# Kernel optimization log

Measured on AMD Instinct MI355X. Metric: run time of the kernel, lower is better.

## Reference

```python
import jax, jax.numpy as jnp
import numpy as np


def _conv(x, w, b, stride, pad):
    y = jax.lax.conv_general_dilated(
        x, w, (stride, stride), [(pad, pad), (pad, pad)],
        dimension_numbers=('NCHW', 'OIHW', 'NCHW'))
    return y + b[None, :, None, None]


def _maxpool(x):
    # kernel 3, stride 2, padding 1 (torch MaxPool2d semantics)
    return jax.lax.reduce_window(
        x, -jnp.inf, jax.lax.max,
        (1, 1, 3, 3), (1, 1, 2, 2), [(0, 0), (0, 0), (1, 1), (1, 1)])


def _squash(s, eps=1e-8):
    n2 = jnp.sum(s * s, axis=-1, keepdims=True)
    return s * (n2 / (1.0 + n2)) / jnp.sqrt(n2 + eps)


def setup_inputs() -> dict:
    key = jax.random.key(0)
    ks = jax.random.split(key, 17)
    s = 0.05
    inp = {
        'x': jax.random.normal(ks[0], (128, 3, 32, 32), jnp.float32),
        'cw1': jax.random.normal(ks[1], (96, 3, 3, 3), jnp.float32) * s,
        'cb1': jnp.zeros((96,), jnp.float32),
        'cw2': jax.random.normal(ks[2], (256, 96, 3, 3), jnp.float32) * s,
        'cb2': jnp.zeros((256,), jnp.float32),
        'cw3': jax.random.normal(ks[3], (384, 256, 3, 3), jnp.float32) * s,
        'cb3': jnp.zeros((384,), jnp.float32),
        'pw': jax.random.normal(ks[4], (256, 384, 3, 3), jnp.float32) * s,  # 32 caps * 8 dim
        'pb': jnp.zeros((256,), jnp.float32),
        'Wcaps': jax.random.normal(ks[5], (100, 1152, 16, 8), jnp.float32) * s,
        'fw1': jax.random.normal(ks[6], (1600, 4096), jnp.float32) * s,
        'fb1': jnp.zeros((4096,), jnp.float32),
        'fw2': jax.random.normal(ks[7], (4096, 4096), jnp.float32) * s,
        'fb2': jnp.zeros((4096,), jnp.float32),
        'fw3': jax.random.normal(ks[8], (4096, 100), jnp.float32) * s,
        'fb3': jnp.zeros((100,), jnp.float32),
    }
    return inp


def reference(x, cw1, cb1, cw2, cb2, cw3, cb3, pw, pb, Wcaps,
              fw1, fb1, fw2, fb2, fw3, fb3):
    ROUTINGS = 3
    # AlexNet-style conv backbone
    h = jax.nn.relu(_conv(x, cw1, cb1, 1, 1))   # [B,96,32,32]
    h = _maxpool(h)                              # [B,96,16,16]
    h = jax.nn.relu(_conv(h, cw2, cb2, 1, 1))   # [B,256,16,16]
    h = _maxpool(h)                              # [B,256,8,8]
    h = jax.nn.relu(_conv(h, cw3, cb3, 1, 1))   # [B,384,8,8]
    # PrimaryCaps: conv 384 -> 32*8, k3 s1 p0 -> [B,256,6,6]
    p = _conv(h, pw, pb, 1, 0)
    u = _squash(p.reshape(p.shape[0], -1, 8))   # [B,1152,8]
    # DenseCapsule: x_hat[b,o,i,d] = sum_e W[o,i,d,e] * u[b,i,e]
    x_hat = jnp.einsum('oide,bie->boid', Wcaps, u)  # [B,100,1152,16]
    x_hat_d = jax.lax.stop_gradient(x_hat)
    b = jnp.zeros(x_hat.shape[:3], x_hat.dtype)     # [B,100,1152]
    v = None
    for r in range(ROUTINGS):
        c = jax.nn.softmax(b, axis=1)               # couple over out caps
        if r == ROUTINGS - 1:
            v = _squash(jnp.einsum('boi,boid->bod', c, x_hat))
        else:
            v = _squash(jnp.einsum('boi,boid->bod', c, x_hat_d))
            b = b + jnp.einsum('boid,bod->boi', x_hat_d, v)
    # Flatten + FC head (dropout is identity at eval)
    f = v.reshape(v.shape[0], -1)                   # [B,1600]
    f = jax.nn.relu(f @ fw1 + fb1)
    f = jax.nn.relu(f @ fw2 + fb2)
    return f @ fw3 + fb3                            # [B,100]
```

## Files before the change

kernel.cpp:

```cpp
#include <hip/hip_runtime.h>
#include <cstddef>


typedef __attribute__((ext_vector_type(8))) short bf8_t;
typedef __attribute__((ext_vector_type(4))) float f4_t;

__device__ inline void cvt_hilo8(const float* f, unsigned* h, unsigned* l)
{
  #pragma unroll
  for (int j = 0; j < 4; ++j) {
    unsigned u0 = __float_as_uint(f[2 * j]);
    unsigned u1 = __float_as_uint(f[2 * j + 1]);
    h[j] = (u0 >> 16) | (u1 & 0xFFFF0000u);
    float r0 = f[2 * j]     - __uint_as_float(u0 & 0xFFFF0000u);
    float r1 = f[2 * j + 1] - __uint_as_float(u1 & 0xFFFF0000u);
    l[j] = (__float_as_uint(r0) >> 16) | (__float_as_uint(r1) & 0xFFFF0000u);
  }
}

__device__ inline void split1(float f, unsigned short& h, unsigned short& l)
{
  unsigned u = __float_as_uint(f);
  h = (unsigned short)(u >> 16);
  float r = f - __uint_as_float(u & 0xFFFF0000u);
  l = (unsigned short)(__float_as_uint(r) >> 16);
}

__device__ inline float bf2f(unsigned short h, unsigned short l)
{
  return __uint_as_float((unsigned)h << 16) + __uint_as_float((unsigned)l << 16);
}

__global__ __launch_bounds__(256) void wsplit_k(
    const float* __restrict__ w, unsigned short* __restrict__ oh,
    unsigned short* __restrict__ ol, int CO, int CI)
{
  int idx = blockIdx.x * 256 + threadIdx.x;
  int ci = idx % CI;
  int t2 = idx / CI;
  int r = t2 % 9, co = t2 / 9;
  float f = w[((size_t)co * CI + ci) * 9 + r];
  unsigned short h, l;
  split1(f, h, l);
  oh[idx] = h; ol[idx] = l;
}

__global__ __launch_bounds__(256) void conv1_k(
    const float* __restrict__ x, const float* __restrict__ wt,
    const float* __restrict__ bias, unsigned short* __restrict__ oh,
    unsigned short* __restrict__ ol)
{
  int idx = blockIdx.x * 256 + threadIdx.x;
  int w = idx & 31, h = (idx >> 5) & 31, b = idx >> 10;
  int co0 = blockIdx.y * 24;

  float xv[27];
  const float* xb = x + (size_t)b * 3072;
  #pragma unroll
  for (int ci = 0; ci < 3; ++ci)
    #pragma unroll
    for (int dh = 0; dh < 3; ++dh) {
      int ih = h + dh - 1;
      #pragma unroll
      for (int dw = 0; dw < 3; ++dw) {
        int iw = w + dw - 1;
        bool ok = ((unsigned)ih < 32u) & ((unsigned)iw < 32u);
        xv[ci * 9 + dh * 3 + dw] = ok ? xb[(ci << 10) + (ih << 5) + iw] : 0.f;
      }
    }

  size_t obase = ((size_t)b * 1024 + (h << 5) + w) * 96 + co0;
  const float* wp = wt + (size_t)co0 * 27;
  #pragma unroll 2
  for (int cp = 0; cp < 12; ++cp) {
    float a0 = bias[co0 + 2 * cp], a1 = bias[co0 + 2 * cp + 1];
    #pragma unroll
    for (int k = 0; k < 27; ++k) {
      a0 += xv[k] * wp[(2 * cp) * 27 + k];
      a1 += xv[k] * wp[(2 * cp + 1) * 27 + k];
    }
    a0 = fmaxf(a0, 0.f); a1 = fmaxf(a1, 0.f);
    unsigned short h0, l0, h1, l1;
    split1(a0, h0, l0); split1(a1, h1, l1);
    *(unsigned*)(oh + obase + 2 * cp) = (unsigned)h0 | ((unsigned)h1 << 16);
    *(unsigned*)(ol + obase + 2 * cp) = (unsigned)l0 | ((unsigned)l1 << 16);
  }
}

template <int C, int H>
__global__ __launch_bounds__(256) void maxpool_bf(
    const unsigned short* __restrict__ inh, const unsigned short* __restrict__ inl,
    unsigned short* __restrict__ outh, unsigned short* __restrict__ outl)
{
  constexpr int Ho = H >> 1;
  int idx = blockIdx.x * 256 + threadIdx.x;
  int c = idx % C;
  int q = idx / C;
  int wo = q % Ho;
  int q2 = q / Ho;
  int ho = q2 % Ho, b = q2 / Ho;
  float best = -3.4e38f;
  unsigned short bh = 0, bl = 0;
  #pragma unroll
  for (int dh = 0; dh < 3; ++dh) {
    int ih = 2 * ho - 1 + dh;
    if ((unsigned)ih >= (unsigned)H) continue;
    #pragma unroll
    for (int dw = 0; dw < 3; ++dw) {
      int iw = 2 * wo - 1 + dw;
      if ((unsigned)iw >= (unsigned)H) continue;
      size_t off = ((size_t)(b * H + ih) * H + iw) * C + c;
      unsigned short uh = inh[off], ul = inl[off];
      float f = bf2f(uh, ul);
      if (f > best) { best = f; bh = uh; bl = ul; }
    }
  }
  outh[idx] = bh; outl[idx] = bl;
}

template <int CI, int H, int PAD, int WO, bool SPLIT>
__global__ __launch_bounds__(256) void convgemm_nhwc(
    const unsigned short* __restrict__ inh, const unsigned short* __restrict__ inl,
    const unsigned short* __restrict__ wh, const unsigned short* __restrict__ wl,
    const float* __restrict__ bias, unsigned short* __restrict__ outh,
    unsigned short* __restrict__ outl, float* __restrict__ outf,
    int CO, int relu, int KC)
{
  constexpr int K = CI * 9;
  constexpr int NPIX = WO * WO;
  __shared__ uint4 Ah[256], Al[256], Bh[256], Bl[256];
  int n0 = blockIdx.x * 64, m0 = blockIdx.y * 64;
  int kbeg = SPLIT ? blockIdx.z * KC : 0;
  int kend = SPLIT ? kbeg + KC : K;
  int t = threadIdx.x;
  int lane = t & 63;
  int wave = __builtin_amdgcn_readfirstlane(t >> 6);
  int wm = wave & 1, wn = wave >> 1;
  int lr = lane & 15, lq = lane >> 4;

  int nn = m0 + lane;
  int bpix = nn / NPIX, xy = nn - bpix * NPIX;
  int ho = xy / WO, wo = xy - ho * WO;
  int ih0 = ho - PAD, iw0 = wo - PAD;
  size_t ibase = (size_t)bpix * H * H;

  uint4 a_h, a_l, b_h, b_l;
  auto loadA = [&](int k0) {
    int kk = k0 + wave * 8;
    int r = kk / CI, ci0 = kk - r * CI;
    int dh = r / 3, dw = r - dh * 3;
    int ih = ih0 + dh, iw = iw0 + dw;
    bool ok = ((unsigned)ih < (unsigned)H) & ((unsigned)iw < (unsigned)H);
    if (ok) {
      size_t ad = ((ibase + (size_t)ih * H + iw) * CI + ci0);
      a_h = *(const uint4*)(inh + ad);
      a_l = *(const uint4*)(inl + ad);
    } else {
      a_h = make_uint4(0u, 0u, 0u, 0u);
      a_l = make_uint4(0u, 0u, 0u, 0u);
    }
  };
  auto loadB = [&](int k0) {
    int kk = k0 + wave * 8;
    size_t ad = (size_t)(n0 + lane) * K + kk;
    b_h = *(const uint4*)(wh + ad);
    b_l = *(const uint4*)(wl + ad);
  };

  loadA(kbeg); loadB(kbeg);
  f4_t acc[2][2];
  #pragma unroll
  for (int mt = 0; mt < 2; ++mt)
    #pragma unroll
    for (int nt = 0; nt < 2; ++nt) acc[mt][nt] = (f4_t)0.0f;

  for (int k0 = kbeg; k0 < kend; k0 += 32) {
    if (k0 > kbeg) __syncthreads();
    Ah[t] = a_h; Al[t] = a_l; Bh[t] = b_h; Bl[t] = b_l;
    __syncthreads();
    if (k0 + 32 < kend) { loadA(k0 + 32); loadB(k0 + 32); }
    bf8_t av_h[2], av_l[2], bv_h[2], bv_l[2];
    #pragma unroll
    for (int mt = 0; mt < 2; ++mt) {
      int ui = lq * 64 + wm * 32 + mt * 16 + lr;
      av_h[mt] = *(const bf8_t*)&Ah[ui];
      av_l[mt] = *(const bf8_t*)&Al[ui];
    }
    #pragma unroll
    for (int nt = 0; nt < 2; ++nt) {
      int ui = lq * 64 + wn * 32 + nt * 16 + lr;
      bv_h[nt] = *(const bf8_t*)&Bh[ui];
      bv_l[nt] = *(const bf8_t*)&Bl[ui];
    }
    #pragma unroll
    for (int mt = 0; mt < 2; ++mt)
      #pragma unroll
      for (int nt = 0; nt < 2; ++nt) {
        acc[mt][nt] = __builtin_amdgcn_mfma_f32_16x16x32_bf16(av_h[mt], bv_h[nt], acc[mt][nt], 0, 0, 0);
        acc[mt][nt] = __builtin_amdgcn_mfma_f32_16x16x32_bf16(av_h[mt], bv_l[nt], acc[mt][nt], 0, 0, 0);
        acc[mt][nt] = __builtin_amdgcn_mfma_f32_16x16x32_bf16(av_l[mt], bv_h[nt], acc[mt][nt], 0, 0, 0);
      }
  }
  #pragma unroll
  for (int mt = 0; mt < 2; ++mt)
    #pragma unroll
    for (int nt = 0; nt < 2; ++nt) {
      #pragma unroll
      for (int r = 0; r < 4; ++r) {
        int m = m0 + wm * 32 + mt * 16 + lq * 4 + r;
        int n = n0 + wn * 32 + nt * 16 + lr;
        size_t oidx = (size_t)m * CO + n;
        if (SPLIT) {
          atomicAdd(outf + oidx, acc[mt][nt][r]);
        } else {
          float vv = acc[mt][nt][r] + bias[n];
          if (relu) vv = fmaxf(vv, 0.f);
          unsigned short h, l;
          split1(vv, h, l);
          outh[oidx] = h; outl[oidx] = l;
        }
      }
    }
}

__global__ __launch_bounds__(256) void fc_mfma(
    const float* __restrict__ A, const float* __restrict__ W,
    float* __restrict__ C, int K, int N, int KC)
{
  __shared__ uint4 Ah[256], Al[256], Bh[256], Bl[256];
  int n0 = blockIdx.x * 64, m0 = blockIdx.y * 64;
  int kbeg = blockIdx.z * KC, kend = kbeg + KC;
  int t = threadIdx.x;
  int lane = t & 63;
  int wave = __builtin_amdgcn_readfirstlane(t >> 6);
  int wm = wave & 1, wn = wave >> 1;
  int lr = lane & 15, lq = lane >> 4;
  int smA = t >> 2, sgA = t & 3;

  float fa[8], fb[8];
  auto loadA = [&](int k0) {
    const float4* ap = (const float4*)(A + (size_t)(m0 + smA) * K + k0 + sgA * 8);
    float4 a0 = ap[0], a1 = ap[1];
    fa[0] = a0.x; fa[1] = a0.y; fa[2] = a0.z; fa[3] = a0.w;
    fa[4] = a1.x; fa[5] = a1.y; fa[6] = a1.z; fa[7] = a1.w;
  };
  auto loadB = [&](int k0) {
    const float* wp = W + (size_t)(k0 + wave * 8) * N + n0 + lane;
    #pragma unroll
    for (int j = 0; j < 8; ++j) fb[j] = wp[(size_t)j * N];
  };

  loadA(kbeg); loadB(kbeg);
  f4_t acc[2][2];
  #pragma unroll
  for (int mt = 0; mt < 2; ++mt)
    #pragma unroll
    for (int nt = 0; nt < 2; ++nt) acc[mt][nt] = (f4_t)0.0f;

  for (int k0 = kbeg; k0 < kend; k0 += 32) {
    if (k0 > kbeg) __syncthreads();
    unsigned ha[4], la[4], hb[4], lb[4];
    cvt_hilo8(fa, ha, la);
    cvt_hilo8(fb, hb, lb);
    Ah[sgA * 64 + smA] = make_uint4(ha[0], ha[1], ha[2], ha[3]);
    Al[sgA * 64 + smA] = make_uint4(la[0], la[1], la[2], la[3]);
    Bh[wave * 64 + lane] = make_uint4(hb[0], hb[1], hb[2], hb[3]);
    Bl[wave * 64 + lane] = make_uint4(lb[0], lb[1], lb[2], lb[3]);
    __syncthreads();
    if (k0 + 32 < kend) { loadA(k0 + 32); loadB(k0 + 32); }
    bf8_t av_h[2], av_l[2], bv_h[2], bv_l[2];
    #pragma unroll
    for (int mt = 0; mt < 2; ++mt) {
      int ui = lq * 64 + wm * 32 + mt * 16 + lr;
      av_h[mt] = *(const bf8_t*)&Ah[ui];
      av_l[mt] = *(const bf8_t*)&Al[ui];
    }
    #pragma unroll
    for (int nt = 0; nt < 2; ++nt) {
      int ui = lq * 64 + wn * 32 + nt * 16 + lr;
      bv_h[nt] = *(const bf8_t*)&Bh[ui];
      bv_l[nt] = *(const bf8_t*)&Bl[ui];
    }
    #pragma unroll
    for (int mt = 0; mt < 2; ++mt)
      #pragma unroll
      for (int nt = 0; nt < 2; ++nt) {
        acc[mt][nt] = __builtin_amdgcn_mfma_f32_16x16x32_bf16(av_h[mt], bv_h[nt], acc[mt][nt], 0, 0, 0);
        acc[mt][nt] = __builtin_amdgcn_mfma_f32_16x16x32_bf16(av_h[mt], bv_l[nt], acc[mt][nt], 0, 0, 0);
        acc[mt][nt] = __builtin_amdgcn_mfma_f32_16x16x32_bf16(av_l[mt], bv_h[nt], acc[mt][nt], 0, 0, 0);
      }
  }
  #pragma unroll
  for (int mt = 0; mt < 2; ++mt)
    #pragma unroll
    for (int nt = 0; nt < 2; ++nt) {
      #pragma unroll
      for (int r = 0; r < 4; ++r) {
        int m = m0 + wm * 32 + mt * 16 + lq * 4 + r;
        int n = n0 + wn * 32 + nt * 16 + lr;
        atomicAdd(C + (size_t)m * N + n, acc[mt][nt][r]);
      }
    }
}

__global__ __launch_bounds__(256) void squash8_k(
    const float* __restrict__ p, const float* __restrict__ pb,
    float* __restrict__ ut)
{
  int idx = blockIdx.x * 256 + threadIdx.x;
  if (idx >= 147456) return;
  int b = idx & 127, i = idx >> 7;
  float pv[8];
  #pragma unroll
  for (int e = 0; e < 8; ++e) {
    int f = i * 8 + e;
    int co = f / 36, pix = f - co * 36;
    pv[e] = p[((size_t)b * 36 + pix) * 256 + co] + pb[co];
  }
  float n2 = 0.f;
  #pragma unroll
  for (int e = 0; e < 8; ++e) n2 += pv[e] * pv[e];
  float sc = (n2 / (1.f + n2)) * rsqrtf(n2 + 1e-8f);
  #pragma unroll
  for (int e = 0; e < 8; ++e)
    ut[(size_t)i * 1024 + e * 128 + b] = pv[e] * sc;
}

__global__ __launch_bounds__(256) void caps_squash16(
    const float* __restrict__ s, float* __restrict__ v, float* __restrict__ vt)
{
  int idx = blockIdx.x * 256 + threadIdx.x;
  if (idx >= 12800) return;
  int b = idx / 100, o = idx % 100;
  const float4* sp = (const float4*)(s + (size_t)idx * 16);
  float4 a = sp[0], bb = sp[1], c = sp[2], d = sp[3];
  float n2 = a.x * a.x + a.y * a.y + a.z * a.z + a.w * a.w +
             bb.x * bb.x + bb.y * bb.y + bb.z * bb.z + bb.w * bb.w +
             c.x * c.x + c.y * c.y + c.z * c.z + c.w * c.w +
             d.x * d.x + d.y * d.y + d.z * d.z + d.w * d.w;
  float sc = (n2 / (1.f + n2)) * rsqrtf(n2 + 1e-8f);
  float vv[16] = {a.x, a.y, a.z, a.w, bb.x, bb.y, bb.z, bb.w,
                  c.x, c.y, c.z, c.w, d.x, d.y, d.z, d.w};
  float4* vp = (float4*)(v + (size_t)idx * 16);
  float4 o0 = {vv[0] * sc, vv[1] * sc, vv[2] * sc, vv[3] * sc};
  float4 o1 = {vv[4] * sc, vv[5] * sc, vv[6] * sc, vv[7] * sc};
  float4 o2 = {vv[8] * sc, vv[9] * sc, vv[10] * sc, vv[11] * sc};
  float4 o3 = {vv[12] * sc, vv[13] * sc, vv[14] * sc, vv[15] * sc};
  vp[0] = o0; vp[1] = o1; vp[2] = o2; vp[3] = o3;
  #pragma unroll
  for (int dd = 0; dd < 16; ++dd)
    vt[((size_t)o * 16 + dd) * 128 + b] = vv[dd] * sc;
}

__global__ __launch_bounds__(256) void caps_spass_mfma(
    const float* __restrict__ W, const float* __restrict__ ut,
    const float* __restrict__ ct, float* __restrict__ s, int uniform)
{
  __shared__ uint4 Ah[512], Al[512];
  int o = blockIdx.x, ks = blockIdx.y;
  int t = threadIdx.x;
  int lane = t & 63;
  int wave = __builtin_amdgcn_readfirstlane(t >> 6);
  int lr = lane & 15, lq = lane >> 4;
  int b = t & 127, half = t >> 7;
  int i0 = ks * 144;

  float fu[16], fc[2], fw[8];
  auto loadUC = [&](int j) {
    int ib = i0 + j * 4 + half * 2;
    #pragma unroll
    for (int q = 0; q < 2; ++q) {
      int i = ib + q;
      #pragma unroll
      for (int e = 0; e < 8; ++e)
        fu[q * 8 + e] = ut[(size_t)i * 1024 + e * 128 + b];
      fc[q] = uniform ? 0.01f : ct[((size_t)o * 1152 + i) * 128 + b];
    }
  };
  auto loadW = [&](int j) {
    int i = i0 + j * 4 + lq;
    const float4* wp = (const float4*)(W + (((size_t)o * 1152 + i) * 16 + lr) * 8);
    float4 w0 = wp[0], w1 = wp[1];
    fw[0] = w0.x; fw[1] = w0.y; fw[2] = w0.z; fw[3] = w0.w;
    fw[4] = w1.x; fw[5] = w1.y; fw[6] = w1.z; fw[7] = w1.w;
  };

  loadUC(0); loadW(0);
  f4_t acc[2];
  acc[0] = (f4_t)0.0f; acc[1] = (f4_t)0.0f;

  for (int j = 0; j < 36; ++j) {
    float cu[16];
    #pragma unroll
    for (int q = 0; q < 2; ++q)
      #pragma unroll
      for (int e = 0; e < 8; ++e)
        cu[q * 8 + e] = fc[q] * fu[q * 8 + e];
    unsigned h0[4], l0[4], h1[4], l1[4], wh[4], wl[4];
    cvt_hilo8(cu, h0, l0);
    cvt_hilo8(cu + 8, h1, l1);
    cvt_hilo8(fw, wh, wl);
    uint4 uwh = make_uint4(wh[0], wh[1], wh[2], wh[3]);
    uint4 uwl = make_uint4(wl[0], wl[1], wl[2], wl[3]);
    bf8_t bfh = *(const bf8_t*)&uwh;
    bf8_t bfl = *(const bf8_t*)&uwl;
    if (j > 0) __syncthreads();
    Ah[(half * 2 + 0) * 128 + b] = make_uint4(h0[0], h0[1], h0[2], h0[3]);
    Al[(half * 2 + 0) * 128 + b] = make_uint4(l0[0], l0[1], l0[2], l0[3]);
    Ah[(half * 2 + 1) * 128 + b] = make_uint4(h1[0], h1[1], h1[2], h1[3]);
    Al[(half * 2 + 1) * 128 + b] = make_uint4(l1[0], l1[1], l1[2], l1[3]);
    __syncthreads();
    if (j + 1 < 36) { loadUC(j + 1); loadW(j + 1); }
    #pragma unroll
    for (int mt = 0; mt < 2; ++mt) {
      int bidx = wave * 16 + mt * 64 + lr;
      bf8_t avh = *(const bf8_t*)&Ah[lq * 128 + bidx];
      bf8_t avl = *(const bf8_t*)&Al[lq * 128 + bidx];
      acc[mt] = __builtin_amdgcn_mfma_f32_16x16x32_bf16(avh, bfh, acc[mt], 0, 0, 0);
      acc[mt] = __builtin_amdgcn_mfma_f32_16x16x32_bf16(avh, bfl, acc[mt], 0, 0, 0);
      acc[mt] = __builtin_amdgcn_mfma_f32_16x16x32_bf16(avl, bfh, acc[mt], 0, 0, 0);
    }
  }
  #pragma unroll
  for (int mt = 0; mt < 2; ++mt)
    #pragma unroll
    for (int r = 0; r < 4; ++r) {
      int bb = wave * 16 + mt * 64 + lq * 4 + r;
      atomicAdd(s + ((size_t)bb * 100 + o) * 16 + lr, acc[mt][r]);
    }
}

__global__ __launch_bounds__(256) void caps_bupdate(
    const float* __restrict__ W, const float* __restrict__ ut,
    const float* __restrict__ vt, float* __restrict__ blogt, int accum)
{
  __shared__ __align__(16) float Wt[64 * 160];
  int o = blockIdx.x, ic = blockIdx.y;
  int t = threadIdx.x;
  int lane = t & 63;
  int wave = __builtin_amdgcn_readfirstlane(t >> 6);
  int lr = lane & 15, lq = lane >> 4;
  int dhalf = (lq & 1) << 3;
  int hl = lq >> 1;

  {
    const float4* Wg = (const float4*)(W + ((size_t)o * 1152 + (size_t)ic * 64) * 128);
    for (int l = t; l < 2048; l += 256) {
      float4 w = Wg[l];
      int li = l >> 5;
      int rem = l & 31;
      int d = rem >> 1;
      int e0 = (rem & 1) << 2;
      float* dst = &Wt[li * 160 + e0 * 20 + d];
      dst[0] = w.x; dst[20] = w.y; dst[40] = w.z; dst[60] = w.w;
    }
  }

  bf8_t B1[8], B2[8];
  #pragma unroll
  for (int nt = 0; nt < 8; ++nt) {
    int b = nt * 16 + lr;
    float vv[8];
    #pragma unroll
    for (int j = 0; j < 8; ++j)
      vv[j] = vt[((size_t)o * 16 + dhalf + j) * 128 + b];
    unsigned h[4], l2[4];
    cvt_hilo8(vv, h, l2);
    uint4 uh = make_uint4(h[0], h[1], h[2], h[3]);
    uint4 ul = (lq < 2) ? make_uint4(l2[0], l2[1], l2[2], l2[3])
                        : make_uint4(0u, 0u, 0u, 0u);
    B1[nt] = *(const bf8_t*)&uh;
    B2[nt] = *(const bf8_t*)&ul;
  }
  __syncthreads();

  unsigned lomask = hl ? 0xFFFF0000u : 0u;

  for (int mi = 0; mi < 8; ++mi) {
    int mt = wave * 8 + mi;
    int liA = mt * 2 + (lr >> 3);
    int eA = lr & 7;
    const float* wp = &Wt[liA * 160 + eA * 20 + dhalf];
    float4 wa = *(const float4*)wp;
    float4 wb = *(const float4*)(wp + 4);
    float fw[8] = {wa.x, wa.y, wa.z, wa.w, wb.x, wb.y, wb.z, wb.w};
    unsigned ha[4];
    #pragma unroll
    for (int j = 0; j < 4; ++j) {
      float f0 = fw[2 * j], f1 = fw[2 * j + 1];
      f0 -= __uint_as_float(__float_as_uint(f0) & lomask);
      f1 -= __uint_as_float(__float_as_uint(f1) & lomask);
      ha[j] = (__float_as_uint(f0) >> 16) | (__float_as_uint(f1) & 0xFFFF0000u);
    }
    uint4 ua = make_uint4(ha[0], ha[1], ha[2], ha[3]);
    bf8_t A = *(const bf8_t*)&ua;

    int gi = ic * 64 + mt * 2 + hl;
    const float* up = ut + (size_t)gi * 1024 + (size_t)(((lq & 1) << 2)) * 128;
    #pragma unroll
    for (int nt = 0; nt < 8; ++nt) {
      f4_t acc = (f4_t)0.0f;
      acc = __builtin_amdgcn_mfma_f32_16x16x32_bf16(A, B1[nt], acc, 0, 0, 0);
      acc = __builtin_amdgcn_mfma_f32_16x16x32_bf16(A, B2[nt], acc, 0, 0, 0);
      int b = nt * 16 + lr;
      float p = acc[0] * up[b] + acc[1] * up[128 + b] +
                acc[2] * up[256 + b] + acc[3] * up[384 + b];
      p += __shfl_xor(p, 16);
      if (!(lq & 1)) {
        size_t off = ((size_t)o * 1152 + gi) * 128 + b;
        if (accum) blogt[off] += p; else blogt[off] = p;
      }
    }
  }
}

__global__ __launch_bounds__(256) void caps_softmax(
    const float* __restrict__ blogt, float* __restrict__ ct)
{
  int idx = blockIdx.x * 256 + threadIdx.x;
  if (idx >= 147456) return;
  const float* bp = blogt + idx;
  float m = -3.4e38f;
  for (int o = 0; o < 100; ++o) m = fmaxf(m, bp[(size_t)o * 147456]);
  float sum = 0.f;
  for (int o = 0; o < 100; ++o) sum += __expf(bp[(size_t)o * 147456] - m);
  float inv = 1.f / sum;
  for (int o = 0; o < 100; ++o)
    ct[(size_t)o * 147456 + idx] = __expf(bp[(size_t)o * 147456] - m) * inv;
}

__global__ __launch_bounds__(256) void bias_act_k(
    float* __restrict__ C, const float* __restrict__ bias, int N, int total, int relu)
{
  int idx = blockIdx.x * 256 + threadIdx.x;
  if (idx >= total) return;
  float vv = C[idx] + bias[idx % N];
  if (relu) vv = fmaxf(vv, 0.f);
  C[idx] = vv;
}

__global__ __launch_bounds__(128) void fc3_seed(
    const float* __restrict__ bias, float* __restrict__ out)
{
  int idx = blockIdx.x * 128 + threadIdx.x;
  if (idx < 12800) out[idx] = bias[idx % 100];
}

__global__ __launch_bounds__(128) void fc3_sk(
    const float* __restrict__ A, const float* __restrict__ W,
    float* __restrict__ out)
{
  __shared__ float Al[1024];
  int m = blockIdx.x, z = blockIdx.y, t = threadIdx.x;
  int kbeg = z * 1024;
  const float* ap = A + (size_t)m * 4096 + kbeg;
  for (int l = t; l < 1024; l += 128) Al[l] = ap[l];
  __syncthreads();
  if (t < 100) {
    float acc = 0.f;
    const float* wp = W + (size_t)kbeg * 100 + t;
    #pragma unroll 8
    for (int k = 0; k < 1024; ++k) acc += Al[k] * wp[(size_t)k * 100];
    atomicAdd(out + m * 100 + t, acc);
  }
}

extern "C" void kernel_launch(void* const* d_in, const int* in_sizes, int n_in,
                              void* d_out, int out_size, void* d_ws, size_t ws_size,
                              hipStream_t stream)
{
  (void)in_sizes; (void)n_in; (void)out_size; (void)ws_size;
  const float* x   = (const float*)d_in[0];
  const float* cw1 = (const float*)d_in[1];
  const float* cb1 = (const float*)d_in[2];
  const float* cw2 = (const float*)d_in[3];
  const float* cb2 = (const float*)d_in[4];
  const float* cw3 = (const float*)d_in[5];
  const float* cb3 = (const float*)d_in[6];
  const float* pw  = (const float*)d_in[7];
  const float* pb  = (const float*)d_in[8];
  const float* Wc  = (const float*)d_in[9];
  const float* fw1 = (const float*)d_in[10];
  const float* fb1 = (const float*)d_in[11];
  const float* fw2 = (const float*)d_in[12];
  const float* fb2 = (const float*)d_in[13];
  const float* fw3 = (const float*)d_in[14];
  const float* fb3 = (const float*)d_in[15];
  float* ws = (float*)d_ws;

  const size_t OFF_A  = 0;
  const size_t OFF_B  = 12582912;
  const size_t OFF_U  = 15728640;
  const size_t OFF_P  = 16908288;
  const size_t OFF_C  = 18087936;
  const size_t OFF_V  = 32833536;
  const size_t OFF_S  = 33038336;
  const size_t OFF_F1 = 33243136;
  const size_t OFF_F2 = 33767424;

  float* ut    = ws + OFF_U;
  float* p     = ws + OFF_P;
  float* vt    = ws + OFF_P;
  float* ct    = ws + OFF_C;
  float* v     = ws + OFF_V;
  float* s     = ws + OFF_S;
  float* f1    = ws + OFF_F1;
  float* f2    = ws + OFF_F2;
  float* blogt = ws + OFF_A;

  unsigned short* h1h  = (unsigned short*)(ws + OFF_A);
  unsigned short* h1l  = h1h + 12582912;
  unsigned short* mp1h = (unsigned short*)(ws + OFF_B);
  unsigned short* mp1l = mp1h + 3145728;
  unsigned short* h2h  = (unsigned short*)(ws + OFF_A);
  unsigned short* h2l  = h2h + 8388608;
  unsigned short* mp2h = (unsigned short*)(ws + OFF_B);
  unsigned short* mp2l = mp2h + 2097152;
  unsigned short* h3h  = (unsigned short*)(ws + OFF_A);
  unsigned short* h3l  = h3h + 3145728;

  unsigned short* wc2h = (unsigned short*)(ws + OFF_C);
  unsigned short* wc2l = wc2h + 221184;
  unsigned short* wc3h = wc2l + 221184;
  unsigned short* wc3l = wc3h + 884736;
  unsigned short* pwth = wc3l + 884736;
  unsigned short* pwtl = pwth + 884736;

  hipMemsetAsync(p,  0, (size_t)1179648 * 4, stream);
  hipMemsetAsync(f1, 0, (size_t)524288 * 4, stream);
  hipMemsetAsync(f2, 0, (size_t)524288 * 4, stream);

  wsplit_k<<<864, 256, 0, stream>>>(cw2, wc2h, wc2l, 256, 96);
  wsplit_k<<<3456, 256, 0, stream>>>(cw3, wc3h, wc3l, 384, 256);
  wsplit_k<<<3456, 256, 0, stream>>>(pw,  pwth, pwtl, 256, 384);

  conv1_k<<<dim3(512, 4), 256, 0, stream>>>(x, cw1, cb1, h1h, h1l);
  maxpool_bf<96, 32><<<12288, 256, 0, stream>>>(h1h, h1l, mp1h, mp1l);
  convgemm_nhwc<96, 16, 1, 16, false><<<dim3(4, 512), 256, 0, stream>>>(
      mp1h, mp1l, wc2h, wc2l, cb2, h2h, h2l, nullptr, 256, 1, 0);
  maxpool_bf<256, 16><<<8192, 256, 0, stream>>>(h2h, h2l, mp2h, mp2l);
  convgemm_nhwc<256, 8, 1, 8, false><<<dim3(6, 128), 256, 0, stream>>>(
      mp2h, mp2l, wc3h, wc3l, cb3, h3h, h3l, nullptr, 384, 1, 0);
  convgemm_nhwc<384, 8, 0, 6, true><<<dim3(4, 72, 2), 256, 0, stream>>>(
      h3h, h3l, pwth, pwtl, pb, nullptr, nullptr, p, 256, 0, 1728);
  squash8_k<<<576, 256, 0, stream>>>(p, pb, ut);

  for (int r = 0; r < 3; ++r) {
    hipMemsetAsync(s, 0, (size_t)204800 * 4, stream);
    if (r == 0) {
      caps_spass_mfma<<<dim3(100, 8), 256, 0, stream>>>(Wc, ut, ut , s, 1);
    } else {
      caps_softmax<<<576, 256, 0, stream>>>(blogt, ct);
      caps_spass_mfma<<<dim3(100, 8), 256, 0, stream>>>(Wc, ut, ct, s, 0);
    }
    caps_squash16<<<50, 256, 0, stream>>>(s, v, vt);
    if (r < 2)
      caps_bupdate<<<dim3(100, 18), 256, 0, stream>>>(Wc, ut, vt, blogt, r);
  }

  fc_mfma<<<dim3(64, 2, 2), 256, 0, stream>>>(v,  fw1, f1, 1600, 4096, 800);
  bias_act_k<<<2048, 256, 0, stream>>>(f1, fb1, 4096, 524288, 1);
  fc_mfma<<<dim3(64, 2, 4), 256, 0, stream>>>(f1, fw2, f2, 4096, 4096, 1024);
  bias_act_k<<<2048, 256, 0, stream>>>(f2, fb2, 4096, 524288, 1);
  fc3_seed<<<100, 128, 0, stream>>>(fb3, (float*)d_out);
  fc3_sk<<<dim3(128, 4), 128, 0, stream>>>(f2, fw3, (float*)d_out);
}
```

Measured before the change: 1.131 ms.

## Enlarge conv GEMM tiles to 128x128 with XCD swizzle and swizzled LDS

Replaces the 64x64-tile implicit-GEMM conv kernel with a 128x128 tile version where each wave computes a 4x4 grid of MFMA tiles. This raises arithmetic intensity per LDS load. It also adds an XOR-swizzled LDS layout to avoid bank conflicts and a block-id remap so neighbouring tiles land on the same XCD for L2 reuse. The split-K for the primary caps conv goes from 2 to 4 chunks. Fewer blocks and higher register use may cut occupancy, and the smaller grids (192, 288 blocks) may underfill the 256 CUs.

```diff
diff --git a/kernel.cpp b/kernel.cpp
--- a/kernel.cpp
+++ b/kernel.cpp
@@ -29,6 +29,13 @@
 __device__ inline float bf2f(unsigned short h, unsigned short l)
 {
   return __uint_as_float((unsigned)h << 16) + __uint_as_float((unsigned)l << 16);
+}
+
+__device__ inline int xcd_swz(int bid, int nwg)
+{
+  int xcd = bid & 7, pos = bid >> 3;
+  int q = nwg >> 3, r = nwg & 7;
+  return (xcd < r ? xcd * (q + 1) : r * (q + 1) + (xcd - r) * q) + pos;
 }
 
 __global__ __launch_bounds__(256) void wsplit_k(
@@ -118,97 +125,119 @@
   outh[idx] = bh; outl[idx] = bl;
 }
 
-template <int CI, int H, int PAD, int WO, bool SPLIT>
-__global__ __launch_bounds__(256) void convgemm_nhwc(
+template <int CI, int H, int PAD, int WO, int CO, int MT, bool SPLIT>
+__global__ __launch_bounds__(256) void conv128(
     const unsigned short* __restrict__ inh, const unsigned short* __restrict__ inl,
     const unsigned short* __restrict__ wh, const unsigned short* __restrict__ wl,
     const float* __restrict__ bias, unsigned short* __restrict__ outh,
     unsigned short* __restrict__ outl, float* __restrict__ outf,
-    int CO, int relu, int KC)
+    int relu, int KC)
 {
   constexpr int K = CI * 9;
   constexpr int NPIX = WO * WO;
-  __shared__ uint4 Ah[256], Al[256], Bh[256], Bl[256];
-  int n0 = blockIdx.x * 64, m0 = blockIdx.y * 64;
+  __shared__ uint4 Ah[512], Al[512], Bh[512], Bl[512];
+
+  int id = xcd_swz(blockIdx.x, gridDim.x);
+  int ntile = id / MT, mtile = id - ntile * MT;
+  int n0 = ntile * 128, m0 = mtile * 128;
   int kbeg = SPLIT ? blockIdx.z * KC : 0;
   int kend = SPLIT ? kbeg + KC : K;
+
   int t = threadIdx.x;
   int lane = t & 63;
   int wave = __builtin_amdgcn_readfirstlane(t >> 6);
   int wm = wave & 1, wn = wave >> 1;
   int lr = lane & 15, lq = lane >> 4;
 
-  int nn = m0 + lane;
-  int bpix = nn / NPIX, xy = nn - bpix * NPIX;
-  int ho = xy / WO, wo = xy - ho * WO;
-  int ih0 = ho - PAD, iw0 = wo - PAD;
-  size_t ibase = (size_t)bpix * H * H;
-
-  uint4 a_h, a_l, b_h, b_l;
+  int srow = (t >> 2) & 63;
+  int kc8 = (t & 3) * 8;
+  int sidx = srow * 4 + ((t & 3) ^ (srow & 3));
+
+  int ih0g[2], iw0g[2];
+  size_t ibaseg[2];
+  #pragma unroll
+  for (int g = 0; g < 2; ++g) {
+    int pix = m0 + g * 64 + srow;
+    int bpix = pix / NPIX, xy = pix - bpix * NPIX;
+    int ho = xy / WO, wo = xy - ho * WO;
+    ih0g[g] = ho - PAD; iw0g[g] = wo - PAD;
+    ibaseg[g] = (size_t)bpix * H * H;
+  }
+
+  uint4 pah[2], pal_[2], pbh[2], pbl[2];
   auto loadA = [&](int k0) {
-    int kk = k0 + wave * 8;
-    int r = kk / CI, ci0 = kk - r * CI;
+    int r = k0 / CI;
+    int cib = k0 - r * CI + kc8;
     int dh = r / 3, dw = r - dh * 3;
-    int ih = ih0 + dh, iw = iw0 + dw;
-    bool ok = ((unsigned)ih < (unsigned)H) & ((unsigned)iw < (unsigned)H);
-    if (ok) {
-      size_t ad = ((ibase + (size_t)ih * H + iw) * CI + ci0);
-      a_h = *(const uint4*)(inh + ad);
-      a_l = *(const uint4*)(inl + ad);
-    } else {
-      a_h = make_uint4(0u, 0u, 0u, 0u);
-      a_l = make_uint4(0u, 0u, 0u, 0u);
+    #pragma unroll
+    for (int g = 0; g < 2; ++g) {
+      int ih = ih0g[g] + dh, iw = iw0g[g] + dw;
+      bool ok = ((unsigned)ih < (unsigned)H) & ((unsigned)iw < (unsigned)H);
+      if (ok) {
+        size_t ad = (ibaseg[g] + (size_t)ih * H + iw) * CI + cib;
+        pah[g] = *(const uint4*)(inh + ad);
+        pal_[g] = *(const uint4*)(inl + ad);
+      } else {
+        pah[g] = make_uint4(0u, 0u, 0u, 0u);
+        pal_[g] = make_uint4(0u, 0u, 0u, 0u);
+      }
     }
   };
   auto loadB = [&](int k0) {
-    int kk = k0 + wave * 8;
-    size_t ad = (size_t)(n0 + lane) * K + kk;
-    b_h = *(const uint4*)(wh + ad);
-    b_l = *(const uint4*)(wl + ad);
+    #pragma unroll
+    for (int g = 0; g < 2; ++g) {
+      size_t ad = (size_t)(n0 + g * 64 + srow) * K + k0 + kc8;
+      pbh[g] = *(const uint4*)(wh + ad);
+      pbl[g] = *(const uint4*)(wl + ad);
+    }
   };
 
   loadA(kbeg); loadB(kbeg);
-  f4_t acc[2][2];
-  #pragma unroll
-  for (int mt = 0; mt < 2; ++mt)
-    #pragma unroll
-    for (int nt = 0; nt < 2; ++nt) acc[mt][nt] = (f4_t)0.0f;
+  f4_t acc[4][4];
+  #pragma unroll
+  for (int mt = 0; mt < 4; ++mt)
+    #pragma unroll
+    for (int nt = 0; nt < 4; ++nt) acc[mt][nt] = (f4_t)0.0f;
 
   for (int k0 = kbeg; k0 < kend; k0 += 32) {
     if (k0 > kbeg) __syncthreads();
-    Ah[t] = a_h; Al[t] = a_l; Bh[t] = b_h; Bl[t] = b_l;
+    Ah[sidx] = pah[0]; Ah[256 + sidx] = pah[1];
+    Al[sidx] = pal_[0]; Al[256 + sidx] = pal_[1];
+    Bh[sidx] = pbh[0]; Bh[256 + sidx] = pbh[1];
+    Bl[sidx] = pbl[0]; Bl[256 + sidx] = pbl[1];
     __syncthreads();
     if (k0 + 32 < kend) { loadA(k0 + 32); loadB(k0 + 32); }
-    bf8_t av_h[2], av_l[2], bv_h[2], bv_l[2];
-    #pragma unroll
-    for (int mt = 0; mt < 2; ++mt) {
-      int ui = lq * 64 + wm * 32 + mt * 16 + lr;
-      av_h[mt] = *(const bf8_t*)&Ah[ui];
-      av_l[mt] = *(const bf8_t*)&Al[ui];
-    }
-    #pragma unroll
-    for (int nt = 0; nt < 2; ++nt) {
-      int ui = lq * 64 + wn * 32 + nt * 16 + lr;
-      bv_h[nt] = *(const bf8_t*)&Bh[ui];
-      bv_l[nt] = *(const bf8_t*)&Bl[ui];
-    }
-    #pragma unroll
-    for (int mt = 0; mt < 2; ++mt)
+
+    int xk = lq ^ (lr & 3);
+    int aBase = wm * 256 + lr * 4 + xk;
+    int bBase = wn * 256 + lr * 4 + xk;
+    bf8_t bvh[4], bvl[4];
+    #pragma unroll
+    for (int nt = 0; nt < 4; ++nt) {
+      bvh[nt] = *(const bf8_t*)&Bh[bBase + nt * 64];
+      bvl[nt] = *(const bf8_t*)&Bl[bBase + nt * 64];
+    }
+    #pragma unroll
+    for (int mt = 0; mt < 4; ++mt) {
+      bf8_t avh = *(const bf8_t*)&Ah[aBase + mt * 64];
+      bf8_t avl = *(const bf8_t*)&Al[aBase + mt * 64];
       #pragma unroll
-      for (int nt = 0; nt < 2; ++nt) {
-        acc[mt][nt] = __builtin_amdgcn_mfma_f32_16x16x32_bf16(av_h[mt], bv_h[nt], acc[mt][nt], 0, 0, 0);
-        acc[mt][nt] = __builtin_amdgcn_mfma_f32_16x16x32_bf16(av_h[mt], bv_l[nt], acc[mt][nt], 0, 0, 0);
-        acc[mt][nt] = __builtin_amdgcn_mfma_f32_16x16x32_bf16(av_l[mt], bv_h[nt], acc[mt][nt], 0, 0, 0);
+      for (int nt = 0; nt < 4; ++nt) {
+        acc[mt][nt] = __builtin_amdgcn_mfma_f32_16x16x32_bf16(avh, bvh[nt], acc[mt][nt], 0, 0, 0);
+        acc[mt][nt] = __builtin_amdgcn_mfma_f32_16x16x32_bf16(avh, bvl[nt], acc[mt][nt], 0, 0, 0);
+        acc[mt][nt] = __builtin_amdgcn_mfma_f32_16x16x32_bf16(avl, bvh[nt], acc[mt][nt], 0, 0, 0);
       }
-  }
-  #pragma unroll
-  for (int mt = 0; mt < 2; ++mt)
-    #pragma unroll
-    for (int nt = 0; nt < 2; ++nt) {
+    }
+  }
+
+  #pragma unroll
+  for (int mt = 0; mt < 4; ++mt)
+    #pragma unroll
+    for (int nt = 0; nt < 4; ++nt) {
       #pragma unroll
       for (int r = 0; r < 4; ++r) {
-        int m = m0 + wm * 32 + mt * 16 + lq * 4 + r;
-        int n = n0 + wn * 32 + nt * 16 + lr;
+        int m = m0 + wm * 64 + mt * 16 + lq * 4 + r;
+        int n = n0 + wn * 64 + nt * 16 + lr;
         size_t oidx = (size_t)m * CO + n;
         if (SPLIT) {
           atomicAdd(outf + oidx, acc[mt][nt][r]);
@@ -636,13 +665,13 @@
 
   conv1_k<<<dim3(512, 4), 256, 0, stream>>>(x, cw1, cb1, h1h, h1l);
   maxpool_bf<96, 32><<<12288, 256, 0, stream>>>(h1h, h1l, mp1h, mp1l);
-  convgemm_nhwc<96, 16, 1, 16, false><<<dim3(4, 512), 256, 0, stream>>>(
-      mp1h, mp1l, wc2h, wc2l, cb2, h2h, h2l, nullptr, 256, 1, 0);
+  conv128<96, 16, 1, 16, 256, 256, false><<<512, 256, 0, stream>>>(
+      mp1h, mp1l, wc2h, wc2l, cb2, h2h, h2l, nullptr, 1, 0);
   maxpool_bf<256, 16><<<8192, 256, 0, stream>>>(h2h, h2l, mp2h, mp2l);
-  convgemm_nhwc<256, 8, 1, 8, false><<<dim3(6, 128), 256, 0, stream>>>(
-      mp2h, mp2l, wc3h, wc3l, cb3, h3h, h3l, nullptr, 384, 1, 0);
-  convgemm_nhwc<384, 8, 0, 6, true><<<dim3(4, 72, 2), 256, 0, stream>>>(
-      h3h, h3l, pwth, pwtl, pb, nullptr, nullptr, p, 256, 0, 1728);
+  conv128<256, 8, 1, 8, 384, 64, false><<<192, 256, 0, stream>>>(
+      mp2h, mp2l, wc3h, wc3l, cb3, h3h, h3l, nullptr, 1, 0);
+  conv128<384, 8, 0, 6, 256, 36, true><<<dim3(72, 1, 4), 256, 0, stream>>>(
+      h3h, h3l, pwth, pwtl, pb, nullptr, nullptr, p, 0, 864);
   squash8_k<<<576, 256, 0, stream>>>(p, pb, ut);
 
   for (int r = 0; r < 3; ++r) {
```

Measured after the change: 1.115 ms. About the same (-1.3%).
